# Performance work log

Hardware: AMD Instinct MI355X
Metric: run time of the kernel (lower is better)

Reference implementation:

```python
import jax, jax.numpy as jnp
import numpy as np

G_GRAPHS = 10000
K = 17  # keypoints per graph
# COCO-17 skeleton bones
SKEL = np.array([(15,13),(13,11),(16,14),(14,12),(11,12),(5,11),(6,12),(5,6),(5,7),
                 (6,8),(7,9),(8,10),(1,2),(0,1),(0,2),(1,3),(2,4),(3,5),(4,6)], dtype=np.int64)
DIMS = [2, 64, 64, 64, 128, 128, 128, 256, 256, 256]
BN_EPS = 1e-5


def setup_inputs() -> dict:
    key = jax.random.key(0)
    ks = jax.random.split(key, 16)
    N = G_GRAPHS * K
    # per-graph skeleton edges (bidirectional), offset per graph
    e = np.concatenate([SKEL, SKEL[:, ::-1]], axis=0)            # [38,2]
    off = np.arange(G_GRAPHS, dtype=np.int64)[:, None, None] * K
    edges = (e[None, :, :] + off).reshape(-1, 2)                 # [G*38, 2]
    inp = {
        'x': jax.random.normal(ks[0], (N, 2), jnp.float32),
        'att': jax.random.uniform(ks[1], (N, 1), jnp.float32),
        'edge_index': jnp.asarray(edges.T),                      # [2, E] int64->int32 ok
    }
    for i in range(9):
        kw = jax.random.fold_in(ks[2], i)
        scale = 1.0 / np.sqrt(DIMS[i])
        inp[f'W{i+1}'] = (jax.random.normal(kw, (DIMS[i], DIMS[i+1]), jnp.float32) * scale)
        inp[f'b{i+1}'] = jnp.zeros((DIMS[i+1],), jnp.float32)
    inp['fcW'] = jax.random.normal(ks[3], (6, 256, 256), jnp.float32) * (1.0 / 16.0)  # [scale,out,in]
    inp['fcB'] = jnp.zeros((6, 256), jnp.float32)
    inp['bn_gamma'] = jnp.ones((6, 256), jnp.float32)
    inp['bn_beta'] = jnp.zeros((6, 256), jnp.float32)
    inp['bn_rm'] = jnp.zeros((6, 256), jnp.float32)
    inp['bn_rv'] = jnpp if False else jnp.ones((6, 256), jnp.float32)
    return inp


def _forward(x, att, edge_index, Ws, bs, fcW, fcB, bn_gamma, bn_beta, bn_rm, bn_rv):
    N = x.shape[0]
    ar = jnp.arange(N, dtype=edge_index.dtype)
    src = jnp.concatenate([edge_index[0], ar])   # add self-loops (PyG GCNConv default)
    dst = jnp.concatenate([edge_index[1], ar])
    deg = jax.ops.segment_sum(jnp.ones_like(dst, dtype=jnp.float32), dst, num_segments=N)
    dinv = 1.0 / jnp.sqrt(deg)                   # deg >= 1 due to self-loops
    norm = (dinv[src] * dinv[dst])[:, None]      # [E+N, 1]

    h = x
    for W, b in zip(Ws, bs):
        msg = (h @ W)[src] * norm                # gather-linear-scale
        agg = jax.ops.segment_sum(msg, dst, num_segments=N)
        h = jnp.maximum((agg + b) * att, 0.0)    # AttGCNConv * att, then ReLU

    # JRPP pooling: [B, 17, 256] -> [B, 6, 256]
    xg = h.reshape(-1, K, h.shape[-1])
    g1 = xg.mean(axis=1, keepdims=True)
    g2 = jnp.concatenate([xg[:, :11].mean(1, keepdims=True),
                          xg[:, 11:].mean(1, keepdims=True)], axis=1)
    head = xg[:, jnp.array([0, 1, 2, 3, 4])].mean(1, keepdims=True)
    larl = xg[:, jnp.array([5, 7, 9, 12, 14, 16])].mean(1, keepdims=True)
    rall = xg[:, jnp.array([6, 8, 10, 11, 13, 15])].mean(1, keepdims=True)
    pooled = jnp.concatenate([g1, g2, head, larl, rall], axis=1)  # [B, 6, 256]

    # per-scale Linear (torch weight layout [out,in]) + eval-mode BatchNorm1d
    ft = jnp.einsum('bsi,soi->bso', pooled, fcW) + fcB
    fi = (ft - bn_rm) * (bn_gamma / jnp.sqrt(bn_rv + BN_EPS)) + bn_beta
    out = fi.reshape(fi.shape[0], -1)            # [B, 1536]
    # F.normalize(p=2, dim=1)
    nrm = jnp.maximum(jnp.linalg.norm(out, axis=1, keepdims=True), 1e-12)
    return out / nrm


def reference(x, att, edge_index, W1, b1, W2, b2, W3, b3, W4, b4, W5, b5, W6, b6,
              W7, b7, W8, b8, W9, b9, fcW, fcB, bn_gamma, bn_beta, bn_rm, bn_rv):
    Ws = [W1, W2, W3, W4, W5, W6, W7, W8, W9]
    bs = [b1, b2, b3, b4, b5, b6, b7, b8, b9]
    return _forward(x, att, edge_index, Ws, bs, fcW, fcB, bn_gamma, bn_beta, bn_rm, bn_rv)
```

## Files before the change

kernel.cpp:

```cpp
#include <hip/hip_runtime.h>
#include <math.h>


typedef _Float16 f16;
typedef _Float16 v2h __attribute__((ext_vector_type(2)));
typedef _Float16 v4h __attribute__((ext_vector_type(4)));
typedef _Float16 v8h __attribute__((ext_vector_type(8)));
typedef float    v4f __attribute__((ext_vector_type(4)));

namespace {

constexpr int BA[19] = {15,13,16,14,11, 5, 6, 5, 5, 6, 7, 8, 1, 0, 0, 1, 2, 3, 4};
constexpr int BB[19] = {13,11,14,12,12,11,12, 6, 7, 8, 9,10, 2, 1, 2, 3, 4, 5, 6};
constexpr float DINV[17] = {
  0.57735026919f, 0.5f, 0.5f, 0.57735026919f, 0.57735026919f,
  0.44721359550f, 0.44721359550f, 0.57735026919f, 0.57735026919f,
  0.70710678119f, 0.70710678119f, 0.5f, 0.5f,
  0.57735026919f, 0.57735026919f, 0.70710678119f, 0.70710678119f};

__device__ __forceinline__ int hswz(int row, int k){
  return row*256 + (k & ~63) + (((((k>>3)&7) ^ (row&7)))<<3) + (k&7);
}
__device__ __forceinline__ int zswz(int c, int r){
  return c*64 + (r ^ ((c&7)<<3) ^ ((c&8)<<2));
}

__device__ __forceinline__ void ldh2(const f16* p, float* d){
  const v2h v = *(const v2h*)p; d[0]=v[0]; d[1]=v[1];
}

template<int KP, int DOUT>
__device__ __forceinline__ void layer_phase(const f16* __restrict__ src,
    f16* __restrict__ dst, f16* ztw,
    const f16* __restrict__ wp, const float* __restrict__ bias,
    const float (&av3)[3], const v8h (&Bfrag)[3][2],
    int w, int m, int q)
{
  constexpr int NKS = KP/32;
  constexpr int NTW = DOUT/64;
  constexpr int CT_PER = (NTW>=2)?2:1;
  constexpr int NPASS = NTW/CT_PER;

  v4f acc[3][NTW];
  #pragma unroll
  for (int a=0;a<3;++a)
    #pragma unroll
    for (int b=0;b<NTW;++b) acc[a][b] = v4f{0.f,0.f,0.f,0.f};

  #pragma unroll
  for (int ks=0; ks<NKS; ++ks){
    v8h af[3];
    #pragma unroll
    for (int mt=0;mt<3;++mt)
      af[mt] = *(const v8h*)(src + hswz(mt*16+m, ks*32 + q*8));
    #pragma unroll
    for (int nt=0;nt<NTW;++nt){
      const v8h bf = *(const v8h*)(wp + ((((w*NTW+nt)*NKS + ks)*64 + q*16 + m)<<3));
      #pragma unroll
      for (int mt=0;mt<3;++mt)
        acc[mt][nt] = __builtin_amdgcn_mfma_f32_16x16x32_f16(af[mt], bf, acc[mt][nt], 0,0,0);
    }
  }

  #pragma unroll
  for (int p=0;p<NPASS;++p){
    #pragma unroll
    for (int nt2=0;nt2<CT_PER;++nt2){
      #pragma unroll
      for (int mt=0;mt<3;++mt){
        v4h z;
        #pragma unroll
        for (int ii=0;ii<4;++ii) z[ii] = (f16)acc[mt][p*CT_PER+nt2][ii];
        *(v4h*)(ztw + zswz(nt2*16+m, mt*16+q*4)) = z;
      }
    }
    #pragma unroll
    for (int ct2=0;ct2<CT_PER;++ct2){
      const v8h za0 = *(const v8h*)(ztw + zswz(ct2*16+m, q*8));
      const v8h za1 = *(const v8h*)(ztw + zswz(ct2*16+m, 32 + q*8));
      v4f a2[3];
      #pragma unroll
      for (int mt=0;mt<3;++mt) a2[mt] = v4f{0.f,0.f,0.f,0.f};
      #pragma unroll
      for (int mt=0;mt<3;++mt)
        a2[mt] = __builtin_amdgcn_mfma_f32_16x16x32_f16(za0, Bfrag[mt][0], a2[mt], 0,0,0);
      #pragma unroll
      for (int mt=0;mt<3;++mt)
        a2[mt] = __builtin_amdgcn_mfma_f32_16x16x32_f16(za1, Bfrag[mt][1], a2[mt], 0,0,0);
      const int cb = w*(DOUT/4) + (p*CT_PER+ct2)*16 + q*4;
      const v4f b4 = *(const v4f*)(bias + cb);
      #pragma unroll
      for (int mt=0;mt<3;++mt){
        v4h o;
        #pragma unroll
        for (int ii=0;ii<4;++ii)
          o[ii] = (f16)fmaxf((a2[mt][ii] + b4[ii])*av3[mt], 0.f);
        *(v4h*)(dst + hswz(mt*16+m, cb)) = o;
      }
    }
  }
}

}

__global__ void prep_kernel(
    const float* __restrict__ W1, const float* __restrict__ W2,
    const float* __restrict__ W3, const float* __restrict__ W4,
    const float* __restrict__ W5, const float* __restrict__ W6,
    const float* __restrict__ W7, const float* __restrict__ W8,
    const float* __restrict__ W9,
    const float* __restrict__ B1, const float* __restrict__ B2,
    const float* __restrict__ B3, const float* __restrict__ B4,
    const float* __restrict__ B5, const float* __restrict__ B6,
    const float* __restrict__ B7, const float* __restrict__ B8,
    const float* __restrict__ B9,
    const float* __restrict__ fcW, const float* __restrict__ bng,
    const float* __restrict__ bnb, const float* __restrict__ bnrm,
    const float* __restrict__ bnrv, const float* __restrict__ att,
    f16* __restrict__ wt, f16* __restrict__ Ath, f16* __restrict__ fcWh,
    float* __restrict__ bnsc, float* __restrict__ bnsh,
    float* __restrict__ bcat, float* __restrict__ attp, int G)
{
  const int idx = blockIdx.x*blockDim.x + threadIdx.x;
  const int stride = gridDim.x*blockDim.x;
  const float* Ws[9] = {W1,W2,W3,W4,W5,W6,W7,W8,W9};
  const float* Bs[9] = {B1,B2,B3,B4,B5,B6,B7,B8,B9};
  const int DINs[9]  = {2,64,64,64,128,128,128,256,256};
  const int DOUTs[9] = {64,64,64,128,128,128,256,256,256};
  const int KPs[9]   = {32,64,64,64,128,128,128,256,256};
  const int OFFs[9]  = {0,2048,6144,10240,18432,34816,51200,83968,149504};
  const int BOFFs[9] = {0,64,128,192,320,448,576,832,1088};
  for (int l=0;l<9;++l){
    const float* W = Ws[l];
    const int DIN=DINs[l], DOUT=DOUTs[l], KP=KPs[l], NKS=KP>>5;
    f16* dst = wt + OFFs[l];
    const int n = DOUT*KP;
    for (int i=idx;i<n;i+=stride){
      const int jj = i&7, mm = (i>>3)&15, qq = (i>>7)&3, r2 = i>>9;
      const int ks = r2 & (NKS-1), ct = r2 / NKS;
      const int k = ks*32 + qq*8 + jj, c = ct*16 + mm;
      dst[i] = (k<DIN) ? (f16)W[k*DOUT+c] : (f16)0.f;
    }
    for (int i=idx;i<DOUT;i+=stride) bcat[BOFFs[l]+i] = Bs[l][i];
  }
  for (int i=idx;i<48*64;i+=stride){
    const int r = i>>6, j = i&63;
    float v = 0.f;
    if (j < 48 && ((r<24) == (j<24))){
      const int a = (r<24)? r : r-24;
      const int b = (j<24)? j : j-24;
      if (a<17 && b<17){
        bool adj = (a==b);
        #pragma unroll
        for (int e=0;e<19;++e)
          adj = adj || (BA[e]==a && BB[e]==b) || (BA[e]==b && BB[e]==a);
        if (adj) v = DINV[a]*DINV[b];
      }
    }
    Ath[i] = (f16)v;
  }
  for (int i=idx;i<6*65536;i+=stride){
    const int s = i>>16, j = i&65535;
    const int jj = j&7, mm = (j>>3)&15, qq = (j>>7)&3, r2 = j>>9;
    const int ks = r2&7, ct = r2>>3;
    const int k = ks*32 + qq*8 + jj, c = ct*16 + mm;
    fcWh[i] = (f16)fcW[(size_t)s*65536 + c*256 + k];
  }
  for (int i=idx;i<1536;i+=stride){
    const float sc = bng[i] * rsqrtf(bnrv[i] + 1e-5f);
    bnsc[i] = sc; bnsh[i] = bnb[i] - bnrm[i]*sc;
  }
  const int G2 = (G+1)&~1;
  for (int i=idx;i<G2*24;i+=stride){
    const int g = i/24, j = i - g*24;
    attp[i] = (j<17 && g<G) ? att[(size_t)g*17 + j] : 0.f;
  }
}

__global__ __launch_bounds__(256, 2)
void gcn_kernel(const float* __restrict__ x, const f16* __restrict__ wt,
                const f16* __restrict__ Ath, const float* __restrict__ attp,
                const float* __restrict__ bcat,
                f16* __restrict__ pooled, int G)
{
  __shared__ __align__(16) f16 Hb[2][48*256];
  __shared__ __align__(16) f16 Zt[4*2048];
  const int t = threadIdx.x, w = t>>6, lane = t&63;
  const int m = lane&15, q = lane>>4;
  const int g0 = blockIdx.x*2;
  f16* ztw = Zt + w*2048;

  v8h Bfrag[3][2];
  #pragma unroll
  for (int mt=0;mt<3;++mt)
    #pragma unroll
    for (int ks2=0;ks2<2;++ks2)
      Bfrag[mt][ks2] = *(const v8h*)(Ath + (mt*16+m)*64 + ks2*32 + q*8);
  float av3[3];
  #pragma unroll
  for (int mt=0;mt<3;++mt) av3[mt] = attp[g0*24 + mt*16 + m];

  {
    const v8h z8 = {0,0,0,0,0,0,0,0};
    #pragma unroll
    for (int i=0;i<4;++i) *(v8h*)(Zt + t*32 + i*8) = z8;
    const int g = t>>7, kk = t&127;
    if (kk < 32){
      #pragma unroll
      for (int i=0;i<17;++i){
        float v = 0.f;
        if (kk < 2 && g0+g < G) v = x[(size_t)(g0+g)*34 + i*2 + kk];
        Hb[0][hswz(g*24+i, kk)] = (f16)v;
      }
      #pragma unroll
      for (int j=17;j<24;++j) Hb[0][hswz(g*24+j, kk)] = (f16)0.f;
    }
  }
  __syncthreads();

  layer_phase< 32, 64>(Hb[0], Hb[1], ztw, wt+0,      bcat+0,    av3, Bfrag, w, m, q); __syncthreads();
  layer_phase< 64, 64>(Hb[1], Hb[0], ztw, wt+2048,   bcat+64,   av3, Bfrag, w, m, q); __syncthreads();
  layer_phase< 64, 64>(Hb[0], Hb[1], ztw, wt+6144,   bcat+128,  av3, Bfrag, w, m, q); __syncthreads();
  layer_phase< 64,128>(Hb[1], Hb[0], ztw, wt+10240,  bcat+192,  av3, Bfrag, w, m, q); __syncthreads();
  layer_phase<128,128>(Hb[0], Hb[1], ztw, wt+18432,  bcat+320,  av3, Bfrag, w, m, q); __syncthreads();
  layer_phase<128,128>(Hb[1], Hb[0], ztw, wt+34816,  bcat+448,  av3, Bfrag, w, m, q); __syncthreads();
  layer_phase<128,256>(Hb[0], Hb[1], ztw, wt+51200,  bcat+576,  av3, Bfrag, w, m, q); __syncthreads();
  layer_phase<256,256>(Hb[1], Hb[0], ztw, wt+83968,  bcat+832,  av3, Bfrag, w, m, q); __syncthreads();
  layer_phase<256,256>(Hb[0], Hb[1], ztw, wt+149504, bcat+1088, av3, Bfrag, w, m, q); __syncthreads();

  const int g = t>>7, tt = t&127, k0 = tt*2, gg = g0 + g;
  if (gg < G){
    float sA[2]={0,0}, sB[2]={0,0}, sH[2]={0,0}, sL[2]={0,0}, sR[2]={0,0};
    #pragma unroll
    for (int i=0;i<17;++i){
      float hi[2];
      ldh2(&Hb[1][hswz(g*24+i, k0)], hi);
      #pragma unroll
      for (int v=0;v<2;++v){
        if (i<11) sA[v]+=hi[v]; else sB[v]+=hi[v];
        if (i<5)  sH[v]+=hi[v];
        if (i==5||i==7||i==9||i==12||i==14||i==16)  sL[v]+=hi[v];
        if (i==6||i==8||i==10||i==11||i==13||i==15) sR[v]+=hi[v];
      }
    }
    f16* op = pooled + (size_t)gg*1536 + k0;
    v2h o;
    #pragma unroll
    for (int v=0;v<2;++v) o[v]=(f16)((sA[v]+sB[v])*(1.0f/17.0f)); *(v2h*)(op+0*256)=o;
    #pragma unroll
    for (int v=0;v<2;++v) o[v]=(f16)(sA[v]*(1.0f/11.0f));         *(v2h*)(op+1*256)=o;
    #pragma unroll
    for (int v=0;v<2;++v) o[v]=(f16)(sB[v]*(1.0f/6.0f));          *(v2h*)(op+2*256)=o;
    #pragma unroll
    for (int v=0;v<2;++v) o[v]=(f16)(sH[v]*(1.0f/5.0f));          *(v2h*)(op+3*256)=o;
    #pragma unroll
    for (int v=0;v<2;++v) o[v]=(f16)(sL[v]*(1.0f/6.0f));          *(v2h*)(op+4*256)=o;
    #pragma unroll
    for (int v=0;v<2;++v) o[v]=(f16)(sR[v]*(1.0f/6.0f));          *(v2h*)(op+5*256)=o;
  }
}

__global__ __launch_bounds__(256, 3)
void head_kernel(const f16* __restrict__ pooled, const f16* __restrict__ fcWh,
                 const float* __restrict__ fcB, const float* __restrict__ bnsc,
                 const float* __restrict__ bnsh, float* __restrict__ out, int G)
{
  __shared__ __align__(16) f16 Ap[16*1536];
  __shared__ float red[64];
  __shared__ float invn[16];
  const int t = threadIdx.x, w = t>>6, lane = t&63;
  const int m = lane&15, q = lane>>4;
  const int g0 = blockIdx.x*16;
  const int cb = w*64;

  for (int id=t; id<16*192; id+=256){
    const int row = id/192, cc = id - row*192;
    v8h v = v8h{0,0,0,0,0,0,0,0};
    const int gg = g0 + row;
    if (gg < G) v = *(const v8h*)(pooled + (size_t)gg*1536 + cc*8);
    const int pc = (cc & ~7) | ((cc&7) ^ (row&7));
    *(v8h*)(Ap + row*1536 + pc*8) = v;
  }
  __syncthreads();

  v4f acc[6][4];
  #pragma unroll
  for (int s=0;s<6;++s)
    #pragma unroll
    for (int nt=0;nt<4;++nt) acc[s][nt] = v4f{0.f,0.f,0.f,0.f};

  #pragma unroll
  for (int s=0;s<6;++s){
    #pragma unroll
    for (int ks=0; ks<8; ++ks){
      const int c = s*32 + ks*4 + q;
      const v8h af = *(const v8h*)(Ap + m*1536 + ((c & ~7) | ((c&7) ^ (m&7)))*8);
      #pragma unroll
      for (int nt=0;nt<4;++nt){
        const v8h bf = *(const v8h*)(fcWh + (size_t)s*65536 +
                         (((((w*4+nt)*8 + ks)*64) + q*16 + m)<<3));
        acc[s][nt] = __builtin_amdgcn_mfma_f32_16x16x32_f16(af, bf, acc[s][nt], 0,0,0);
      }
    }
  }

  float ss[4] = {0.f,0.f,0.f,0.f};
  #pragma unroll
  for (int s=0;s<6;++s)
    #pragma unroll
    for (int nt=0;nt<4;++nt){
      const int idx = s*256 + cb + nt*16 + m;
      const float bc = fcB[idx], sc = bnsc[idx], sh = bnsh[idx];
      #pragma unroll
      for (int i=0;i<4;++i){
        const float f = (acc[s][nt][i] + bc)*sc + sh;
        acc[s][nt][i] = f;
        ss[i] += f*f;
      }
    }

  #pragma unroll
  for (int off=1; off<16; off<<=1)
    #pragma unroll
    for (int i=0;i<4;++i) ss[i] += __shfl_xor(ss[i], off, 64);
  if (m==0)
    #pragma unroll
    for (int i=0;i<4;++i) red[w*16 + q*4 + i] = ss[i];
  __syncthreads();
  if (t < 16){
    const float s4 = red[t] + red[16+t] + red[32+t] + red[48+t];
    invn[t] = 1.f / fmaxf(sqrtf(s4), 1e-12f);
  }
  __syncthreads();
  float iv[4];
  #pragma unroll
  for (int i=0;i<4;++i) iv[i] = invn[q*4+i];
  #pragma unroll
  for (int s=0;s<6;++s)
    #pragma unroll
    for (int nt=0;nt<4;++nt)
      #pragma unroll
      for (int i=0;i<4;++i){
        const int gg = g0 + q*4 + i;
        if (gg < G)
          out[(size_t)gg*1536 + s*256 + cb + nt*16 + m] = acc[s][nt][i]*iv[i];
      }
}

extern "C" void kernel_launch(void* const* d_in, const int* in_sizes, int n_in,
                              void* d_out, int out_size, void* d_ws, size_t ws_size,
                              hipStream_t stream) {
  (void)n_in; (void)out_size; (void)ws_size;
  const float* x   = (const float*)d_in[0];
  const float* att = (const float*)d_in[1];
  const float* W[9]; const float* B[9];
  for (int i=0;i<9;i++){ W[i]=(const float*)d_in[3+2*i]; B[i]=(const float*)d_in[4+2*i]; }
  const float* fcW  = (const float*)d_in[21];
  const float* fcB  = (const float*)d_in[22];
  const float* bn_g = (const float*)d_in[23];
  const float* bn_b = (const float*)d_in[24];
  const float* bn_rm= (const float*)d_in[25];
  const float* bn_rv= (const float*)d_in[26];
  float* out = (float*)d_out;

  const int G = in_sizes[1] / 17;
  const int G2 = (G+1)&~1;

  char* ws = (char*)d_ws;
  f16*   wt   = (f16*)(ws);
  f16*   fcWh = (f16*)(ws + 430080);
  float* bnsc = (float*)(ws + 1216512);
  float* bnsh = (float*)(ws + 1222656);
  float* bcat = (float*)(ws + 1228800);
  f16*   Ath  = (f16*)(ws + 1234176);
  float* attp = (float*)(ws + 1240320);
  size_t poolOff = (1240320 + (size_t)G2*96 + 255) & ~(size_t)255;
  f16* pooled = (f16*)(ws + poolOff);

  prep_kernel<<<2048, 256, 0, stream>>>(
      W[0],W[1],W[2],W[3],W[4],W[5],W[6],W[7],W[8],
      B[0],B[1],B[2],B[3],B[4],B[5],B[6],B[7],B[8],
      fcW, bn_g, bn_b, bn_rm, bn_rv, att,
      wt, Ath, fcWh, bnsc, bnsh, bcat, attp, G);

  const int gb = (G + 1) / 2;
  gcn_kernel<<<gb, 256, 0, stream>>>(
      x, wt, Ath, attp, bcat, pooled, G);

  head_kernel<<<(G + 15)/16, 256, 0, stream>>>(
      pooled, fcWh, fcB, bnsc, bnsh, out, G);
}
```

Baseline: 344.3 us.

## Process one graph per block with 32-row tiles and two waves

Changes the GCN kernel from two graphs per 256-thread block (48 padded rows, 24 per graph) to one graph per 128-thread block with 32 padded rows. The aggregation matmul drops from a 48x64 block-diagonal adjacency to a single 32x32 adjacency, which cuts the wasted MFMA work on padding rows and the K=64 aggregation step. Each wave now covers twice as many output columns, and shared memory per block shrinks, which should raise occupancy. In exchange there are twice as many blocks, and weight fragments are reused across fewer rows per load.

New measurement: 391.3 us. +13.6%, slower.

```diff
diff --git a/kernel.cpp b/kernel.cpp
--- a/kernel.cpp
+++ b/kernel.cpp
@@ -33,31 +33,30 @@
 __device__ __forceinline__ void layer_phase(const f16* __restrict__ src,
     f16* __restrict__ dst, f16* ztw,
     const f16* __restrict__ wp, const float* __restrict__ bias,
-    const float (&av3)[3], const v8h (&Bfrag)[3][2],
+    const float (&av)[2], const v8h (&Bfrag)[2],
     int w, int m, int q)
 {
   constexpr int NKS = KP/32;
-  constexpr int NTW = DOUT/64;
-  constexpr int CT_PER = (NTW>=2)?2:1;
-  constexpr int NPASS = NTW/CT_PER;
-
-  v4f acc[3][NTW];
-  #pragma unroll
-  for (int a=0;a<3;++a)
+  constexpr int NTW = DOUT/32;
+  constexpr int NPASS = NTW/2;
+
+  v4f acc[2][NTW];
+  #pragma unroll
+  for (int a=0;a<2;++a)
     #pragma unroll
     for (int b=0;b<NTW;++b) acc[a][b] = v4f{0.f,0.f,0.f,0.f};
 
   #pragma unroll
   for (int ks=0; ks<NKS; ++ks){
-    v8h af[3];
-    #pragma unroll
-    for (int mt=0;mt<3;++mt)
+    v8h af[2];
+    #pragma unroll
+    for (int mt=0;mt<2;++mt)
       af[mt] = *(const v8h*)(src + hswz(mt*16+m, ks*32 + q*8));
     #pragma unroll
     for (int nt=0;nt<NTW;++nt){
       const v8h bf = *(const v8h*)(wp + ((((w*NTW+nt)*NKS + ks)*64 + q*16 + m)<<3));
       #pragma unroll
-      for (int mt=0;mt<3;++mt)
+      for (int mt=0;mt<2;++mt)
         acc[mt][nt] = __builtin_amdgcn_mfma_f32_16x16x32_f16(af[mt], bf, acc[mt][nt], 0,0,0);
     }
   }
@@ -65,36 +64,32 @@
   #pragma unroll
   for (int p=0;p<NPASS;++p){
     #pragma unroll
-    for (int nt2=0;nt2<CT_PER;++nt2){
-      #pragma unroll
-      for (int mt=0;mt<3;++mt){
+    for (int ct2=0;ct2<2;++ct2){
+      #pragma unroll
+      for (int mt=0;mt<2;++mt){
+        const v4f a4 = acc[mt][p*2+ct2];
         v4h z;
         #pragma unroll
-        for (int ii=0;ii<4;++ii) z[ii] = (f16)acc[mt][p*CT_PER+nt2][ii];
-        *(v4h*)(ztw + zswz(nt2*16+m, mt*16+q*4)) = z;
-      }
-    }
-    #pragma unroll
-    for (int ct2=0;ct2<CT_PER;++ct2){
-      const v8h za0 = *(const v8h*)(ztw + zswz(ct2*16+m, q*8));
-      const v8h za1 = *(const v8h*)(ztw + zswz(ct2*16+m, 32 + q*8));
-      v4f a2[3];
-      #pragma unroll
-      for (int mt=0;mt<3;++mt) a2[mt] = v4f{0.f,0.f,0.f,0.f};
-      #pragma unroll
-      for (int mt=0;mt<3;++mt)
-        a2[mt] = __builtin_amdgcn_mfma_f32_16x16x32_f16(za0, Bfrag[mt][0], a2[mt], 0,0,0);
-      #pragma unroll
-      for (int mt=0;mt<3;++mt)
-        a2[mt] = __builtin_amdgcn_mfma_f32_16x16x32_f16(za1, Bfrag[mt][1], a2[mt], 0,0,0);
-      const int cb = w*(DOUT/4) + (p*CT_PER+ct2)*16 + q*4;
+        for (int ii=0;ii<4;++ii) z[ii] = (f16)a4[ii];
+        *(v4h*)(ztw + zswz(ct2*16+m, mt*16+q*4)) = z;
+      }
+    }
+    #pragma unroll
+    for (int ct2=0;ct2<2;++ct2){
+      const v8h za = *(const v8h*)(ztw + zswz(ct2*16+m, q*8));
+      const v4f z4 = v4f{0.f,0.f,0.f,0.f};
+      v4f a2[2];
+      #pragma unroll
+      for (int mt=0;mt<2;++mt)
+        a2[mt] = __builtin_amdgcn_mfma_f32_16x16x32_f16(za, Bfrag[mt], z4, 0,0,0);
+      const int cb = w*(DOUT/2) + p*32 + ct2*16 + q*4;
       const v4f b4 = *(const v4f*)(bias + cb);
       #pragma unroll
-      for (int mt=0;mt<3;++mt){
+      for (int mt=0;mt<2;++mt){
         v4h o;
         #pragma unroll
         for (int ii=0;ii<4;++ii)
-          o[ii] = (f16)fmaxf((a2[mt][ii] + b4[ii])*av3[mt], 0.f);
+          o[ii] = (f16)fmaxf((a2[mt][ii] + b4[ii])*av[mt], 0.f);
         *(v4h*)(dst + hswz(mt*16+m, cb)) = o;
       }
     }
@@ -117,7 +112,7 @@
     const float* __restrict__ fcW, const float* __restrict__ bng,
     const float* __restrict__ bnb, const float* __restrict__ bnrm,
     const float* __restrict__ bnrv, const float* __restrict__ att,
-    f16* __restrict__ wt, f16* __restrict__ Ath, f16* __restrict__ fcWh,
+    f16* __restrict__ wt, f16* __restrict__ At32, f16* __restrict__ fcWh,
     float* __restrict__ bnsc, float* __restrict__ bnsh,
     float* __restrict__ bcat, float* __restrict__ attp, int G)
 {
@@ -143,21 +138,17 @@
     }
     for (int i=idx;i<DOUT;i+=stride) bcat[BOFFs[l]+i] = Bs[l][i];
   }
-  for (int i=idx;i<48*64;i+=stride){
-    const int r = i>>6, j = i&63;
+  for (int i=idx;i<32*32;i+=stride){
+    const int r = i>>5, j = i&31;
     float v = 0.f;
-    if (j < 48 && ((r<24) == (j<24))){
-      const int a = (r<24)? r : r-24;
-      const int b = (j<24)? j : j-24;
-      if (a<17 && b<17){
-        bool adj = (a==b);
-        #pragma unroll
-        for (int e=0;e<19;++e)
-          adj = adj || (BA[e]==a && BB[e]==b) || (BA[e]==b && BB[e]==a);
-        if (adj) v = DINV[a]*DINV[b];
-      }
-    }
-    Ath[i] = (f16)v;
+    if (r<17 && j<17){
+      bool adj = (r==j);
+      #pragma unroll
+      for (int e=0;e<19;++e)
+        adj = adj || (BA[e]==r && BB[e]==j) || (BA[e]==j && BB[e]==r);
+      if (adj) v = DINV[r]*DINV[j];
+    }
+    At32[i] = (f16)v;
   }
   for (int i=idx;i<6*65536;i+=stride){
     const int s = i>>16, j = i&65535;
@@ -170,71 +161,62 @@
     const float sc = bng[i] * rsqrtf(bnrv[i] + 1e-5f);
     bnsc[i] = sc; bnsh[i] = bnb[i] - bnrm[i]*sc;
   }
-  const int G2 = (G+1)&~1;
-  for (int i=idx;i<G2*24;i+=stride){
-    const int g = i/24, j = i - g*24;
-    attp[i] = (j<17 && g<G) ? att[(size_t)g*17 + j] : 0.f;
-  }
-}
-
-__global__ __launch_bounds__(256, 2)
+  for (int i=idx;i<G*32;i+=stride){
+    const int g = i>>5, j = i&31;
+    attp[i] = (j<17) ? att[(size_t)g*17 + j] : 0.f;
+  }
+}
+
+__global__ __launch_bounds__(128, 2)
 void gcn_kernel(const float* __restrict__ x, const f16* __restrict__ wt,
-                const f16* __restrict__ Ath, const float* __restrict__ attp,
+                const f16* __restrict__ At32, const float* __restrict__ attp,
                 const float* __restrict__ bcat,
                 f16* __restrict__ pooled, int G)
 {
-  __shared__ __align__(16) f16 Hb[2][48*256];
-  __shared__ __align__(16) f16 Zt[4*2048];
+  __shared__ __align__(16) f16 Hb[2][32*256];
+  __shared__ __align__(16) f16 Zt[2][2048];
   const int t = threadIdx.x, w = t>>6, lane = t&63;
   const int m = lane&15, q = lane>>4;
-  const int g0 = blockIdx.x*2;
-  f16* ztw = Zt + w*2048;
-
-  v8h Bfrag[3][2];
-  #pragma unroll
-  for (int mt=0;mt<3;++mt)
-    #pragma unroll
-    for (int ks2=0;ks2<2;++ks2)
-      Bfrag[mt][ks2] = *(const v8h*)(Ath + (mt*16+m)*64 + ks2*32 + q*8);
-  float av3[3];
-  #pragma unroll
-  for (int mt=0;mt<3;++mt) av3[mt] = attp[g0*24 + mt*16 + m];
+  const int gg = blockIdx.x;
+  f16* ztw = Zt[w];
+
+  v8h Bfrag[2];
+  #pragma unroll
+  for (int mt=0;mt<2;++mt)
+    Bfrag[mt] = *(const v8h*)(At32 + (mt*16+m)*32 + q*8);
+  float av[2];
+  #pragma unroll
+  for (int mt=0;mt<2;++mt) av[mt] = attp[(size_t)gg*32 + mt*16 + m];
 
   {
-    const v8h z8 = {0,0,0,0,0,0,0,0};
-    #pragma unroll
-    for (int i=0;i<4;++i) *(v8h*)(Zt + t*32 + i*8) = z8;
-    const int g = t>>7, kk = t&127;
-    if (kk < 32){
-      #pragma unroll
-      for (int i=0;i<17;++i){
-        float v = 0.f;
-        if (kk < 2 && g0+g < G) v = x[(size_t)(g0+g)*34 + i*2 + kk];
-        Hb[0][hswz(g*24+i, kk)] = (f16)v;
-      }
-      #pragma unroll
-      for (int j=17;j<24;++j) Hb[0][hswz(g*24+j, kk)] = (f16)0.f;
+    const int kk = t&31, rg = t>>5;
+    #pragma unroll
+    for (int r8=0;r8<8;++r8){
+      const int rr = rg*8 + r8;
+      float v = 0.f;
+      if (kk < 2 && rr < 17) v = x[(size_t)gg*34 + rr*2 + kk];
+      Hb[0][hswz(rr, kk)] = (f16)v;
     }
   }
   __syncthreads();
 
-  layer_phase< 32, 64>(Hb[0], Hb[1], ztw, wt+0,      bcat+0,    av3, Bfrag, w, m, q); __syncthreads();
-  layer_phase< 64, 64>(Hb[1], Hb[0], ztw, wt+2048,   bcat+64,   av3, Bfrag, w, m, q); __syncthreads();
-  layer_phase< 64, 64>(Hb[0], Hb[1], ztw, wt+6144,   bcat+128,  av3, Bfrag, w, m, q); __syncthreads();
-  layer_phase< 64,128>(Hb[1], Hb[0], ztw, wt+10240,  bcat+192,  av3, Bfrag, w, m, q); __syncthreads();
-  layer_phase<128,128>(Hb[0], Hb[1], ztw, wt+18432,  bcat+320,  av3, Bfrag, w, m, q); __syncthreads();
-  layer_phase<128,128>(Hb[1], Hb[0], ztw, wt+34816,  bcat+448,  av3, Bfrag, w, m, q); __syncthreads();
-  layer_phase<128,256>(Hb[0], Hb[1], ztw, wt+51200,  bcat+576,  av3, Bfrag, w, m, q); __syncthreads();
-  layer_phase<256,256>(Hb[1], Hb[0], ztw, wt+83968,  bcat+832,  av3, Bfrag, w, m, q); __syncthreads();
-  layer_phase<256,256>(Hb[0], Hb[1], ztw, wt+149504, bcat+1088, av3, Bfrag, w, m, q); __syncthreads();
-
-  const int g = t>>7, tt = t&127, k0 = tt*2, gg = g0 + g;
-  if (gg < G){
+  layer_phase< 32, 64>(Hb[0], Hb[1], ztw, wt+0,      bcat+0,    av, Bfrag, w, m, q); __syncthreads();
+  layer_phase< 64, 64>(Hb[1], Hb[0], ztw, wt+2048,   bcat+64,   av, Bfrag, w, m, q); __syncthreads();
+  layer_phase< 64, 64>(Hb[0], Hb[1], ztw, wt+6144,   bcat+128,  av, Bfrag, w, m, q); __syncthreads();
+  layer_phase< 64,128>(Hb[1], Hb[0], ztw, wt+10240,  bcat+192,  av, Bfrag, w, m, q); __syncthreads();
+  layer_phase<128,128>(Hb[0], Hb[1], ztw, wt+18432,  bcat+320,  av, Bfrag, w, m, q); __syncthreads();
+  layer_phase<128,128>(Hb[1], Hb[0], ztw, wt+34816,  bcat+448,  av, Bfrag, w, m, q); __syncthreads();
+  layer_phase<128,256>(Hb[0], Hb[1], ztw, wt+51200,  bcat+576,  av, Bfrag, w, m, q); __syncthreads();
+  layer_phase<256,256>(Hb[1], Hb[0], ztw, wt+83968,  bcat+832,  av, Bfrag, w, m, q); __syncthreads();
+  layer_phase<256,256>(Hb[0], Hb[1], ztw, wt+149504, bcat+1088, av, Bfrag, w, m, q); __syncthreads();
+
+  {
+    const int k0 = t*2;
     float sA[2]={0,0}, sB[2]={0,0}, sH[2]={0,0}, sL[2]={0,0}, sR[2]={0,0};
     #pragma unroll
     for (int i=0;i<17;++i){
       float hi[2];
-      ldh2(&Hb[1][hswz(g*24+i, k0)], hi);
+      ldh2(&Hb[1][hswz(i, k0)], hi);
       #pragma unroll
       for (int v=0;v<2;++v){
         if (i<11) sA[v]+=hi[v]; else sB[v]+=hi[v];
@@ -364,7 +346,6 @@
   float* out = (float*)d_out;
 
   const int G = in_sizes[1] / 17;
-  const int G2 = (G+1)&~1;
 
   char* ws = (char*)d_ws;
   f16*   wt   = (f16*)(ws);
@@ -372,20 +353,19 @@
   float* bnsc = (float*)(ws + 1216512);
   float* bnsh = (float*)(ws + 1222656);
   float* bcat = (float*)(ws + 1228800);
-  f16*   Ath  = (f16*)(ws + 1234176);
-  float* attp = (float*)(ws + 1240320);
-  size_t poolOff = (1240320 + (size_t)G2*96 + 255) & ~(size_t)255;
+  f16*   At32 = (f16*)(ws + 1234176);
+  float* attp = (float*)(ws + 1236224);
+  size_t poolOff = (1236224 + (size_t)G*128 + 255) & ~(size_t)255;
   f16* pooled = (f16*)(ws + poolOff);
 
   prep_kernel<<<2048, 256, 0, stream>>>(
       W[0],W[1],W[2],W[3],W[4],W[5],W[6],W[7],W[8],
       B[0],B[1],B[2],B[3],B[4],B[5],B[6],B[7],B[8],
       fcW, bn_g, bn_b, bn_rm, bn_rv, att,
-      wt, Ath, fcWh, bnsc, bnsh, bcat, attp, G);
-
-  const int gb = (G + 1) / 2;
-  gcn_kernel<<<gb, 256, 0, stream>>>(
-      x, wt, Ath, attp, bcat, pooled, G);
+      wt, At32, fcWh, bnsc, bnsh, bcat, attp, G);
+
+  gcn_kernel<<<G, 128, 0, stream>>>(
+      x, wt, At32, attp, bcat, pooled, G);
 
   head_kernel<<<(G + 15)/16, 256, 0, stream>>>(
       pooled, fcWh, fcB, bnsc, bnsh, out, G);
```
